# Optimization experiments

Measured on AMD Instinct MI355X. Metric: run time of the kernel, lower is better.

Reference implementation:

```python
import jax, jax.numpy as jnp
import numpy as np
from functools import partial

IMG, P, C, E, DEPTH, H, FE, NCLS = 224, 16, 3, 768, 12, 12, 4, 1000
B = 32
NP = (IMG // P) ** 2          # 196 patches
N = NP + 1                    # +cls token
HD = E // H                   # 64
FF = FE * E                   # 3072
EPS = 1e-5


def setup_inputs() -> dict:
    key = jax.random.key(0)
    ks = iter(jax.random.split(key, 32))
    r = lambda shape, s=0.02: (jax.random.normal(next(ks), shape, jnp.float32) * s)
    inp = {
        "x": jax.random.normal(next(ks), (B, C, IMG, IMG), jnp.float32),
        "conv_w": r((E, C, P, P)),              # OIHW
        "conv_b": r((E,)),
        "cls_token": r((1, 1, E)),
        "pos_emb": r((1, N, E)),
        # stacked per-layer params; Linear weights stored as [in, out]
        "Wq": r((DEPTH, E, E)), "Wk": r((DEPTH, E, E)), "Wv": r((DEPTH, E, E)),
        "Wo": r((DEPTH, E, E)), "bo": r((DEPTH, E)),
        "ln1_g": jnp.ones((DEPTH, E)), "ln1_b": jnp.zeros((DEPTH, E)),
        "W1": r((DEPTH, E, FF)), "b1": r((DEPTH, FF)),
        "W2": r((DEPTH, FF, E)), "b2": r((DEPTH, E)),
        "ln2_g": jnp.ones((DEPTH, E)), "ln2_b": jnp.zeros((DEPTH, E)),
        "head_g": jnp.ones((E,)), "head_b": jnp.zeros((E,)),
        "head_W": r((E, NCLS)), "head_bias": r((NCLS,)),
    }
    return inp


def _ln(x, g, b):
    m = jnp.mean(x, axis=-1, keepdims=True)
    v = jnp.var(x, axis=-1, keepdims=True)
    return (x - m) * jax.lax.rsqrt(v + EPS) * g + b


def _block(h, p):
    Wq, Wk, Wv, Wo, bo, g1, bn1, W1, b1, W2, b2, g2, bn2 = p
    b, n, _ = h.shape
    q = (h @ Wq).reshape(b, n, H, HD)
    k = (h @ Wk).reshape(b, n, H, HD)
    v = (h @ Wv).reshape(b, n, H, HD)
    # NOTE: original scales by sqrt(embed_size), not sqrt(head_dim)
    energy = jnp.einsum("bqhd,bkhd->bhqk", q, k) / jnp.sqrt(jnp.float32(E))
    attn = jax.nn.softmax(energy, axis=-1)
    out = jnp.einsum("bhqk,bkhd->bqhd", attn, v).reshape(b, n, E)
    out = out @ Wo + bo
    x = _ln(out + h, g1, bn1)
    f = jax.nn.relu(x @ W1 + b1) @ W2 + b2
    return _ln(f + x, g2, bn2), None


def reference(x, conv_w, conv_b, cls_token, pos_emb, Wq, Wk, Wv, Wo, bo,
              ln1_g, ln1_b, W1, b1, W2, b2, ln2_g, ln2_b,
              head_g, head_b, head_W, head_bias):
    # patch embedding: strided conv == non-overlapping patch projection
    h = jax.lax.conv_general_dilated(
        x, conv_w, window_strides=(P, P), padding="VALID",
        dimension_numbers=("NCHW", "OIHW", "NCHW"))
    h = h + conv_b[None, :, None, None]
    h = h.reshape(B, E, NP).transpose(0, 2, 1)          # [B, NP, E]
    cls = jnp.broadcast_to(cls_token, (B, 1, E))
    h = jnp.concatenate([cls, h], axis=1) + pos_emb      # [B, N, E]
    params = (Wq, Wk, Wv, Wo, bo, ln1_g, ln1_b, W1, b1, W2, b2, ln2_g, ln2_b)
    h, _ = jax.lax.scan(_block, h, params)
    cls_final = h[:, 0]
    return _ln(cls_final, head_g, head_b) @ head_W + head_bias
```

## Files before the change

kernel.cpp:

```cpp
#include <hip/hip_runtime.h>

#define NTOK 197
#define BATCH 32
#define ROWS (BATCH*NTOK)
#define EMB 768
#define FFDIM 3072
#define NHEAD 12
#define HDIM 64
#define NPAD 224

typedef __bf16 bf16x8_t __attribute__((ext_vector_type(8)));
typedef float f32x4 __attribute__((ext_vector_type(4)));
typedef unsigned short u16;
typedef u16 u16x4 __attribute__((ext_vector_type(4)));

__device__ __forceinline__ u16 f2b(float f) {
  union { float f; unsigned int u; } v; v.f = f;
  unsigned int r = v.u + 0x7fffu + ((v.u >> 16) & 1u);
  return (u16)(r >> 16);
}
__device__ __forceinline__ void gload16(const void* g, void* l) {
  __builtin_amdgcn_global_load_lds((const __attribute__((address_space(1))) void*)g,
                                   (__attribute__((address_space(3))) void*)l, 16, 0, 0);
}
__device__ __forceinline__ float wred_sum(float v) {
#pragma unroll
  for (int o = 32; o > 0; o >>= 1) v += __shfl_xor(v, o);
  return v;
}

__device__ __forceinline__ void xcd_swz(int& bx, int& by) {
  const int gx = gridDim.x;
  const int nwg = gx * gridDim.y;
  const int orig = by * gx + bx;
  const int q = nwg >> 3, r = nwg & 7;
  const int xcd = orig & 7, idx = orig >> 3;
  const int wg = (xcd < r ? xcd * (q + 1) : r * (q + 1) + (xcd - r) * q) + idx;
  by = wg / gx; bx = wg % gx;
}

template <bool HAS_BIAS, bool RELU, bool ADD_RES, bool OUT_BF16>
__global__ __launch_bounds__(256)
void gemm_bt(const u16* __restrict__ A, const u16* __restrict__ Bt, void* __restrict__ C,
             const float* __restrict__ bias, const float* __restrict__ res,
             int M, int N, int K) {
  __shared__ __align__(16) char lds[2][16384];
  const int tid = threadIdx.x;
  const int lane = tid & 63;
  const int wid = tid >> 6;
  const int wm = wid >> 1, wn = wid & 1;
  int bxs = blockIdx.x, bys = blockIdx.y;
  xcd_swz(bxs, bys);
  const int bm = bys * 128, bn = bxs * 128;
  const int r15 = lane & 15, khi = lane >> 4;

  f32x4 acc[4][4] = {};
  const int nk = K >> 5;

  auto stage = [&](int buf, int kt) {
    const int k0 = kt * 32 + khi * 8;
#pragma unroll
    for (int i = 0; i < 4; ++i) {
      int s = wid * 4 + i;
      char* ldst = &lds[buf][s * 1024];
      const u16* g;
      if (s < 8) {
        int row = bm + s * 16 + r15; if (row >= M) row = M - 1;
        g = A + (size_t)row * K + k0;
      } else {
        int row = bn + (s - 8) * 16 + r15;
        g = Bt + (size_t)row * K + k0;
      }
      gload16(g, ldst);
    }
  };

  stage(0, 0);
  __syncthreads();
  for (int kt = 0; kt < nk; ++kt) {
    const int cur = kt & 1;
    if (kt + 1 < nk) stage(cur ^ 1, kt + 1);
    bf16x8_t a[4], b[4];
#pragma unroll
    for (int mt = 0; mt < 4; ++mt)
      a[mt] = *(const bf16x8_t*)&lds[cur][(wm * 4 + mt) * 1024 + lane * 16];
#pragma unroll
    for (int nt = 0; nt < 4; ++nt)
      b[nt] = *(const bf16x8_t*)&lds[cur][8192 + (wn * 4 + nt) * 1024 + lane * 16];
#pragma unroll
    for (int mt = 0; mt < 4; ++mt)
#pragma unroll
      for (int nt = 0; nt < 4; ++nt)
        acc[mt][nt] = __builtin_amdgcn_mfma_f32_16x16x32_bf16(a[mt], b[nt], acc[mt][nt], 0, 0, 0);
    __syncthreads();
  }

#pragma unroll
  for (int mt = 0; mt < 4; ++mt) {
#pragma unroll
    for (int nt = 0; nt < 4; ++nt) {
      const int col = bn + wn * 64 + nt * 16 + r15;
      float bv = 0.f;
      if (HAS_BIAS) bv = bias[col];
#pragma unroll
      for (int j = 0; j < 4; ++j) {
        const int row = bm + wm * 64 + mt * 16 + khi * 4 + j;
        if (row < M) {
          float v = acc[mt][nt][j] + bv;
          if (ADD_RES) v += res[(size_t)row * N + col];
          if (RELU) v = v > 0.f ? v : 0.f;
          if (OUT_BF16) ((u16*)C)[(size_t)row * N + col] = f2b(v);
          else          ((float*)C)[(size_t)row * N + col] = v;
        }
      }
    }
  }
}

template <bool HAS_BIAS, bool RELU, bool OUT_BF16>
__global__ __launch_bounds__(512)
void gemm_bt2(const u16* __restrict__ A, const u16* __restrict__ Bt, void* __restrict__ C,
              const float* __restrict__ bias, int M, int N, int K) {
  __shared__ __align__(16) char lds[2][24576];
  const int tid = threadIdx.x;
  const int lane = tid & 63;
  const int wid = tid >> 6;
  const int wm = wid >> 1, wn = wid & 1;
  int bxs = blockIdx.x, bys = blockIdx.y;
  xcd_swz(bxs, bys);
  const int bm = bys * 256, bn = bxs * 128;
  const int r15 = lane & 15, khi = lane >> 4;

  f32x4 acc[4][4] = {};
  const int nk = K >> 5;

  auto stage = [&](int buf, int kt) {
    const int k0 = kt * 32 + khi * 8;
#pragma unroll
    for (int i = 0; i < 3; ++i) {
      int s = wid * 3 + i;
      char* ldst = &lds[buf][s * 1024];
      const u16* g;
      if (s < 16) {
        int row = bm + s * 16 + r15; if (row >= M) row = M - 1;
        g = A + (size_t)row * K + k0;
      } else {
        int row = bn + (s - 16) * 16 + r15;
        g = Bt + (size_t)row * K + k0;
      }
      gload16(g, ldst);
    }
  };

  stage(0, 0);
  stage(1, 1);
  for (int kt = 0; kt < nk; ++kt) {
    const int cur = kt & 1;
    if (kt + 1 < nk) { asm volatile("s_waitcnt vmcnt(3)" ::: "memory"); }
    else             { asm volatile("s_waitcnt vmcnt(0)" ::: "memory"); }
    __builtin_amdgcn_sched_barrier(0);
    __builtin_amdgcn_s_barrier();
    bf16x8_t a[4], b[4];
#pragma unroll
    for (int mt = 0; mt < 4; ++mt)
      a[mt] = *(const bf16x8_t*)&lds[cur][(wm * 4 + mt) * 1024 + lane * 16];
#pragma unroll
    for (int nt = 0; nt < 4; ++nt)
      b[nt] = *(const bf16x8_t*)&lds[cur][16384 + (wn * 4 + nt) * 1024 + lane * 16];
#pragma unroll
    for (int mt = 0; mt < 4; ++mt)
#pragma unroll
      for (int nt = 0; nt < 4; ++nt)
        acc[mt][nt] = __builtin_amdgcn_mfma_f32_16x16x32_bf16(a[mt], b[nt], acc[mt][nt], 0, 0, 0);
    asm volatile("s_waitcnt lgkmcnt(0)" ::: "memory");
    __builtin_amdgcn_sched_barrier(0);
    __builtin_amdgcn_s_barrier();
    if (kt + 2 < nk) stage(cur, kt + 2);
  }

#pragma unroll
  for (int mt = 0; mt < 4; ++mt) {
#pragma unroll
    for (int nt = 0; nt < 4; ++nt) {
      const int col = bn + wn * 64 + nt * 16 + r15;
      float bv = 0.f;
      if (HAS_BIAS) bv = bias[col];
#pragma unroll
      for (int j = 0; j < 4; ++j) {
        const int row = bm + wm * 64 + mt * 16 + khi * 4 + j;
        if (row < M) {
          float v = acc[mt][nt][j] + bv;
          if (RELU) v = v > 0.f ? v : 0.f;
          if (OUT_BF16) ((u16*)C)[(size_t)row * N + col] = f2b(v);
          else          ((float*)C)[(size_t)row * N + col] = v;
        }
      }
    }
  }
}

template <int NSK>
__global__ __launch_bounds__(256)
void gemm_bt_sk(const u16* __restrict__ A, const u16* __restrict__ Bt,
                float* __restrict__ P0, float* __restrict__ P1, float* __restrict__ P2,
                int M, int N, int K) {
  __shared__ __align__(16) char lds[2][16384];
  const int tid = threadIdx.x;
  const int lane = tid & 63;
  const int wid = tid >> 6;
  const int wm = wid >> 1, wn = wid & 1;
  int bxs = blockIdx.x, bys = blockIdx.y;
  xcd_swz(bxs, bys);
  const int bm = bys * 128, bn = bxs * 128;
  const int r15 = lane & 15, khi = lane >> 4;
  const int Kh = K / NSK;
  const int kbase = blockIdx.z * Kh;
  float* __restrict__ C = (blockIdx.z == 0) ? P0 : (blockIdx.z == 1 ? P1 : P2);

  f32x4 acc[4][4] = {};
  const int nk = Kh >> 5;

  auto stage = [&](int buf, int kt) {
    const int k0 = kbase + kt * 32 + khi * 8;
#pragma unroll
    for (int i = 0; i < 4; ++i) {
      int s = wid * 4 + i;
      char* ldst = &lds[buf][s * 1024];
      const u16* g;
      if (s < 8) {
        int row = bm + s * 16 + r15; if (row >= M) row = M - 1;
        g = A + (size_t)row * K + k0;
      } else {
        int row = bn + (s - 8) * 16 + r15;
        g = Bt + (size_t)row * K + k0;
      }
      gload16(g, ldst);
    }
  };

  stage(0, 0);
  stage(1, 1);
  for (int kt = 0; kt < nk; ++kt) {
    const int cur = kt & 1;
    if (kt + 1 < nk) { asm volatile("s_waitcnt vmcnt(4)" ::: "memory"); }
    else             { asm volatile("s_waitcnt vmcnt(0)" ::: "memory"); }
    __builtin_amdgcn_sched_barrier(0);
    __builtin_amdgcn_s_barrier();
    bf16x8_t a[4], b[4];
#pragma unroll
    for (int mt = 0; mt < 4; ++mt)
      a[mt] = *(const bf16x8_t*)&lds[cur][(wm * 4 + mt) * 1024 + lane * 16];
#pragma unroll
    for (int nt = 0; nt < 4; ++nt)
      b[nt] = *(const bf16x8_t*)&lds[cur][8192 + (wn * 4 + nt) * 1024 + lane * 16];
#pragma unroll
    for (int mt = 0; mt < 4; ++mt)
#pragma unroll
      for (int nt = 0; nt < 4; ++nt)
        acc[mt][nt] = __builtin_amdgcn_mfma_f32_16x16x32_bf16(a[mt], b[nt], acc[mt][nt], 0, 0, 0);
    asm volatile("s_waitcnt lgkmcnt(0)" ::: "memory");
    __builtin_amdgcn_sched_barrier(0);
    __builtin_amdgcn_s_barrier();
    if (kt + 2 < nk) stage(cur, kt + 2);
  }

#pragma unroll
  for (int mt = 0; mt < 4; ++mt) {
#pragma unroll
    for (int nt = 0; nt < 4; ++nt) {
      const int col = bn + wn * 64 + nt * 16 + r15;
#pragma unroll
      for (int j = 0; j < 4; ++j) {
        const int row = bm + wm * 64 + mt * 16 + khi * 4 + j;
        if (row < M) C[(size_t)row * N + col] = acc[mt][nt][j];
      }
    }
  }
}

__global__ __launch_bounds__(256)
void ln_red(const float* __restrict__ P0, const float* __restrict__ P1,
            const float* __restrict__ P2,
            const float* __restrict__ bias, const float* __restrict__ res,
            const float* __restrict__ g, const float* __restrict__ bv,
            float* __restrict__ o32, u16* __restrict__ obf) {
  const int row = blockIdx.x;
  const size_t b4 = (size_t)row * 192;
  const int tid = threadIdx.x;
  f32x4 vv = {0.f, 0.f, 0.f, 0.f};
  float ls = 0.f, lq = 0.f;
  if (tid < 192) {
    f32x4 a = ((const f32x4*)P0)[b4 + tid];
    f32x4 b = ((const f32x4*)P1)[b4 + tid];
    f32x4 p = ((const f32x4*)P2)[b4 + tid];
    f32x4 c = ((const f32x4*)res)[b4 + tid];
    f32x4 d = ((const f32x4*)bias)[tid];
    vv = a + b + p + c + d;
    ls = vv[0] + vv[1] + vv[2] + vv[3];
    lq = vv[0]*vv[0] + vv[1]*vv[1] + vv[2]*vv[2] + vv[3]*vv[3];
  }
  float s = wred_sum(ls);
  float s2 = wred_sum(lq);
  __shared__ float rs[4], rq[4];
  const int wv = tid >> 6, lane = tid & 63;
  if (lane == 0) { rs[wv] = s; rq[wv] = s2; }
  __syncthreads();
  float S1 = rs[0] + rs[1] + rs[2] + rs[3];
  float S2 = rq[0] + rq[1] + rq[2] + rq[3];
  float mean = S1 * (1.0f / 768.0f);
  float var = S2 * (1.0f / 768.0f) - mean * mean;
  float inv = rsqrtf(var + 1e-5f);
  if (tid < 192) {
    f32x4 gg = ((const f32x4*)g)[tid];
    f32x4 bb = ((const f32x4*)bv)[tid];
    f32x4 y;
    u16x4 ob;
#pragma unroll
    for (int k = 0; k < 4; ++k) {
      y[k] = (vv[k] - mean) * inv * gg[k] + bb[k];
      ob[k] = f2b(y[k]);
    }
    ((f32x4*)o32)[b4 + tid] = y;
    ((u16x4*)obf)[b4 + tid] = ob;
  }
}

__global__ void prep_layer(const float* __restrict__ Wq, const float* __restrict__ Wk,
                           const float* __restrict__ Wv, const float* __restrict__ Wo,
                           const float* __restrict__ W1, const float* __restrict__ W2,
                           u16* __restrict__ qkvT, u16* __restrict__ woT,
                           u16* __restrict__ w1T, u16* __restrict__ w2T) {
  __shared__ float tbuf[32][33];
  const int t = blockIdx.x;
  const float* src; u16* dst; int K, N, nt, kt;
  if (t < 2304) {
    int seg = t / 576, r = t % 576;
    nt = r % 24; kt = r / 24; K = 768; N = 768;
    if (seg == 0)      { src = Wq; dst = qkvT; }
    else if (seg == 1) { src = Wk; dst = qkvT + (size_t)768 * 768; }
    else if (seg == 2) { src = Wv; dst = qkvT + (size_t)2 * 768 * 768; }
    else               { src = Wo; dst = woT; }
  } else if (t < 4608) {
    int r = t - 2304; nt = r % 96; kt = r / 96;
    K = 768; N = 3072; src = W1; dst = w1T;
  } else {
    int r = t - 4608; nt = r % 24; kt = r / 24;
    K = 3072; N = 768; src = W2; dst = w2T;
  }
  const int n0 = nt * 32, k0 = kt * 32;
  const int tx = threadIdx.x, ty = threadIdx.y;
#pragma unroll
  for (int i = 0; i < 4; ++i)
    tbuf[ty + i * 8][tx] = src[(size_t)(k0 + ty + i * 8) * N + n0 + tx];
  __syncthreads();
#pragma unroll
  for (int i = 0; i < 4; ++i)
    dst[(size_t)(n0 + ty + i * 8) * K + k0 + tx] = f2b(tbuf[tx][ty + i * 8]);
}

__global__ void convert_bf(const float* __restrict__ s, u16* __restrict__ d, size_t n) {
  size_t i = (size_t)blockIdx.x * 256 + threadIdx.x;
  if (i < n) d[i] = f2b(s[i]);
}

__global__ void transpose_head(const float* __restrict__ src, float* __restrict__ dst) {
  __shared__ float tbuf[32][33];
  const int n0 = blockIdx.x * 32, k0 = blockIdx.y * 32;
  const int tx = threadIdx.x, ty = threadIdx.y;
#pragma unroll
  for (int i = 0; i < 4; ++i) {
    int k = k0 + ty + i * 8, n = n0 + tx;
    if (n < 1000) tbuf[ty + i * 8][tx] = src[(size_t)k * 1000 + n];
  }
  __syncthreads();
#pragma unroll
  for (int i = 0; i < 4; ++i) {
    int n = n0 + ty + i * 8, k = k0 + tx;
    if (n < 1000) dst[(size_t)n * 768 + k] = tbuf[tx][ty + i * 8];
  }
}

__global__ void im2col(const float* __restrict__ x, u16* __restrict__ A) {
  size_t idx = (size_t)blockIdx.x * 256 + threadIdx.x;
  if (idx >= (size_t)6272 * 768) return;
  int k = (int)(idx % 768); size_t row = idx / 768;
  int b = (int)(row / 196), p = (int)(row % 196);
  int py = p / 14, px = p % 14;
  int c = k >> 8, rem = k & 255, ph = rem >> 4, pw = rem & 15;
  float v = x[(((size_t)b * 3 + c) * 224 + (py * 16 + ph)) * 224 + (px * 16 + pw)];
  A[idx] = f2b(v);
}

__global__ void assemble_h0(const float* __restrict__ pout, const float* __restrict__ cls,
                            const float* __restrict__ pos, float* __restrict__ h32,
                            u16* __restrict__ hbf) {
  const int row = blockIdx.x;
  const int b = row / NTOK, n = row % NTOK;
  for (int c = threadIdx.x; c < EMB; c += 256) {
    float v;
    if (n == 0) v = cls[c] + pos[c];
    else v = pout[((size_t)b * 196 + (n - 1)) * EMB + c] + pos[(size_t)n * EMB + c];
    h32[(size_t)row * EMB + c] = v;
    hbf[(size_t)row * EMB + c] = f2b(v);
  }
}

__global__ void build_vT(const u16* __restrict__ qkv, u16* __restrict__ vT) {
  size_t idx = (size_t)blockIdx.x * 256 + threadIdx.x;
  if (idx >= (size_t)384 * HDIM * NPAD) return;
  int nn = (int)(idx % NPAD); size_t t = idx / NPAD;
  int d = (int)(t % HDIM); int bh = (int)(t / HDIM);
  int b = bh / NHEAD, h = bh % NHEAD;
  u16 v = 0;
  if (nn < NTOK) v = qkv[((size_t)b * NTOK + nn) * 2304 + 1536 + h * HDIM + d];
  vT[idx] = v;
}

__global__ __launch_bounds__(256)
void attn_sm(const u16* __restrict__ qkv, u16* __restrict__ P) {
  __shared__ __align__(16) char kf[13 * 2 * 1024];
  __shared__ __align__(16) char qf[2 * 2 * 1024];
  __shared__ float S[32][NPAD];
  const int bh = blockIdx.y;
  const int b = bh / NHEAD, h = bh % NHEAD;
  const int qb = blockIdx.x;
  const int tid = threadIdx.x, lane = tid & 63, wid = tid >> 6;
  const int r15 = lane & 15, khi = lane >> 4;

  const u16* qbase = qkv + (size_t)b * NTOK * 2304 + h * HDIM;
  const u16* kbase = qbase + 768;

  for (int i = wid; i < 26; i += 4) {
    int sub = i >> 1, ks = i & 1;
    int row = sub * 16 + r15; if (row > 196) row = 196;
    gload16(kbase + (size_t)row * 2304 + ks * 32 + khi * 8, &kf[(size_t)i * 1024]);
  }
  {
    int i = wid;
    int sub = i >> 1, ks = i & 1;
    int row = qb * 32 + sub * 16 + r15; if (row > 196) row = 196;
    gload16(qbase + (size_t)row * 2304 + ks * 32 + khi * 8, &qf[(size_t)i * 1024]);
  }
  __syncthreads();

  const float scale = 0.03608439182435161f;
  for (int t = wid; t < 26; t += 4) {
    int qi = t / 13, ki = t % 13;
    f32x4 acc = {};
    bf16x8_t aq0 = *(const bf16x8_t*)&qf[(qi * 2 + 0) * 1024 + lane * 16];
    bf16x8_t aq1 = *(const bf16x8_t*)&qf[(qi * 2 + 1) * 1024 + lane * 16];
    bf16x8_t bk0 = *(const bf16x8_t*)&kf[(ki * 2 + 0) * 1024 + lane * 16];
    bf16x8_t bk1 = *(const bf16x8_t*)&kf[(ki * 2 + 1) * 1024 + lane * 16];
    acc = __builtin_amdgcn_mfma_f32_16x16x32_bf16(aq0, bk0, acc, 0, 0, 0);
    acc = __builtin_amdgcn_mfma_f32_16x16x32_bf16(aq1, bk1, acc, 0, 0, 0);
#pragma unroll
    for (int j = 0; j < 4; ++j) S[qi * 16 + khi * 4 + j][ki * 16 + r15] = acc[j] * scale;
  }
  __syncthreads();

  for (int i = 0; i < 8; ++i) {
    const int r = wid * 8 + i;
    const int q = qb * 32 + r;
    if (q > 196) continue;
    float vals[4]; float m = -1e30f;
#pragma unroll
    for (int c = 0; c < 4; ++c) {
      int col = lane + c * 64;
      float v = (col < NTOK) ? S[r][col] : -1e30f;
      vals[c] = v; m = fmaxf(m, v);
    }
#pragma unroll
    for (int o = 32; o > 0; o >>= 1) m = fmaxf(m, __shfl_xor(m, o));
    float s = 0.f;
#pragma unroll
    for (int c = 0; c < 4; ++c) { float e = __expf(vals[c] - m); vals[c] = e; s += e; }
    s = wred_sum(s);
    float inv = 1.f / s;
    u16* prow = P + ((size_t)bh * NTOK + q) * NPAD;
#pragma unroll
    for (int c = 0; c < 4; ++c) {
      int col = lane + c * 64;
      if (col < NPAD) prow[col] = f2b(vals[c] * inv);
    }
  }
}

__global__ __launch_bounds__(256)
void attn_pv(const u16* __restrict__ P, const u16* __restrict__ vT, u16* __restrict__ out) {
  __shared__ __align__(16) char lds[2][17 * 1024];
  const int bh = blockIdx.x;
  const int b = bh / NHEAD, h = bh % NHEAD;
  const int tid = threadIdx.x, lane = tid & 63, wid = tid >> 6;
  const int r15 = lane & 15, khi = lane >> 4;
  const u16* Pb = P + (size_t)bh * NTOK * NPAD;
  const u16* Vb = vT + (size_t)bh * HDIM * NPAD;

  f32x4 acc[4][4] = {};
  auto stage = [&](int buf, int kt) {
    for (int i = wid; i < 17; i += 4) {
      const u16* g;
      if (i < 13) { int row = i * 16 + r15; if (row > 196) row = 196;
                    g = Pb + (size_t)row * NPAD + kt * 32 + khi * 8; }
      else        { int row = (i - 13) * 16 + r15;
                    g = Vb + (size_t)row * NPAD + kt * 32 + khi * 8; }
      gload16(g, &lds[buf][i * 1024]);
    }
  };
  stage(0, 0);
  __syncthreads();
  for (int kt = 0; kt < 7; ++kt) {
    const int cur = kt & 1;
    if (kt + 1 < 7) stage(cur ^ 1, kt + 1);
    bf16x8_t bb[4];
#pragma unroll
    for (int di = 0; di < 4; ++di)
      bb[di] = *(const bf16x8_t*)&lds[cur][(13 + di) * 1024 + lane * 16];
#pragma unroll
    for (int s = 0; s < 4; ++s) {
      int qi = wid + s * 4;
      if (qi < 13) {
        bf16x8_t a = *(const bf16x8_t*)&lds[cur][qi * 1024 + lane * 16];
#pragma unroll
        for (int di = 0; di < 4; ++di)
          acc[s][di] = __builtin_amdgcn_mfma_f32_16x16x32_bf16(a, bb[di], acc[s][di], 0, 0, 0);
      }
    }
    __syncthreads();
  }
#pragma unroll
  for (int s = 0; s < 4; ++s) {
    int qi = wid + s * 4;
    if (qi >= 13) continue;
#pragma unroll
    for (int di = 0; di < 4; ++di) {
      int col = h * HDIM + di * 16 + r15;
#pragma unroll
      for (int j = 0; j < 4; ++j) {
        int q = qi * 16 + khi * 4 + j;
        if (q < NTOK) out[((size_t)b * NTOK + q) * EMB + col] = f2b(acc[s][di][j]);
      }
    }
  }
}

__global__ __launch_bounds__(256)
void ln_cls(const float* __restrict__ h32, const float* __restrict__ hg,
            const float* __restrict__ hb, float* __restrict__ cls_ln) {
  const int b = blockIdx.x;
  const float* xr = h32 + (size_t)b * NTOK * EMB;
  const int tid = threadIdx.x;
  float v0 = xr[tid], v1 = xr[tid + 256], v2 = xr[tid + 512];
  float s = wred_sum(v0 + v1 + v2);
  float s2 = wred_sum(v0 * v0 + v1 * v1 + v2 * v2);
  __shared__ float rs[4], rq[4];
  const int wid = tid >> 6, lane = tid & 63;
  if (lane == 0) { rs[wid] = s; rq[wid] = s2; }
  __syncthreads();
  float S1 = rs[0] + rs[1] + rs[2] + rs[3];
  float S2 = rq[0] + rq[1] + rq[2] + rq[3];
  float mean = S1 * (1.0f / 768.0f);
  float var = S2 * (1.0f / 768.0f) - mean * mean;
  float inv = rsqrtf(var + 1e-5f);
  cls_ln[(size_t)b * EMB + tid]       = (v0 - mean) * inv * hg[tid]       + hb[tid];
  cls_ln[(size_t)b * EMB + tid + 256] = (v1 - mean) * inv * hg[tid + 256] + hb[tid + 256];
  cls_ln[(size_t)b * EMB + tid + 512] = (v2 - mean) * inv * hg[tid + 512] + hb[tid + 512];
}

__global__ __launch_bounds__(256)
void head2(const float* __restrict__ cls_ln, const float* __restrict__ hWT,
           const float* __restrict__ bias, float* __restrict__ out) {
  __shared__ float t[EMB];
  const int b = blockIdx.y;
  const int tid = threadIdx.x, lane = tid & 63, wid = tid >> 6;
  t[tid] = cls_ln[(size_t)b * EMB + tid];
  t[tid + 256] = cls_ln[(size_t)b * EMB + tid + 256];
  t[tid + 512] = cls_ln[(size_t)b * EMB + tid + 512];
  __syncthreads();
  const int j = blockIdx.x * 4 + wid;
  const float* wr = hWT + (size_t)j * EMB;
  float a = 0.f;
#pragma unroll
  for (int i = 0; i < 12; ++i) {
    int e = lane + i * 64;
    a += t[e] * wr[e];
  }
  a = wred_sum(a);
  if (lane == 0) out[(size_t)b * 1000 + j] = a + bias[j];
}

extern "C" void kernel_launch(void* const* d_in, const int* in_sizes, int n_in,
                              void* d_out, int out_size, void* d_ws, size_t ws_size,
                              hipStream_t stream) {
  const float* x      = (const float*)d_in[0];
  const float* conv_w = (const float*)d_in[1];
  const float* conv_b = (const float*)d_in[2];
  const float* cls    = (const float*)d_in[3];
  const float* pos    = (const float*)d_in[4];
  const float* Wq     = (const float*)d_in[5];
  const float* Wk     = (const float*)d_in[6];
  const float* Wv     = (const float*)d_in[7];
  const float* Wo     = (const float*)d_in[8];
  const float* bo     = (const float*)d_in[9];
  const float* ln1g   = (const float*)d_in[10];
  const float* ln1b   = (const float*)d_in[11];
  const float* W1     = (const float*)d_in[12];
  const float* b1     = (const float*)d_in[13];
  const float* W2     = (const float*)d_in[14];
  const float* b2     = (const float*)d_in[15];
  const float* ln2g   = (const float*)d_in[16];
  const float* ln2b   = (const float*)d_in[17];
  const float* hg     = (const float*)d_in[18];
  const float* hb     = (const float*)d_in[19];
  const float* hW     = (const float*)d_in[20];
  const float* hbias  = (const float*)d_in[21];

  char* ws = (char*)d_ws;
  size_t off = 0;
  auto alloc = [&](size_t bytes) { void* p = ws + off; off += (bytes + 255) & ~(size_t)255; return p; };

  u16*   qkvT = (u16*)alloc((size_t)2304 * 768 * 2);
  u16*   woTl = (u16*)alloc((size_t)768 * 768 * 2);
  u16*   w1Tl = (u16*)alloc((size_t)3072 * 768 * 2);
  u16*   w2Tl = (u16*)alloc((size_t)768 * 3072 * 2);
  u16*   cw   = (u16*)alloc((size_t)768 * 768 * 2);
  float* h32  = (float*)alloc((size_t)ROWS * EMB * 4);
  u16*   hbf  = (u16*)alloc((size_t)ROWS * EMB * 2);
  u16*   qkv  = (u16*)alloc((size_t)ROWS * 2304 * 2);
  u16*   vT   = (u16*)alloc((size_t)384 * HDIM * NPAD * 2);
  char*  big  = (char*)alloc(2 * (size_t)ROWS * EMB * 4);
  u16*   Pbuf = (u16*)big;
  u16*   mid  = (u16*)big;
  float* pout = (float*)big;
  float* woP0 = (float*)big;
  float* woP1 = (float*)(big + (size_t)ROWS * EMB * 4);
  u16*   att  = (u16*)alloc((size_t)ROWS * EMB * 2);
  u16*   xbf  = att;
  float* ybuf = (float*)alloc((size_t)ROWS * EMB * 4);
  float* x32  = (float*)alloc((size_t)ROWS * EMB * 4);
  float* hWT  = (float*)alloc((size_t)1000 * EMB * 4);
  float* clsl = (float*)alloc((size_t)32 * EMB * 4);
  u16*   Apatch = qkv;
  float* woP2 = ybuf;
  float* f2P0 = (float*)qkv;
  float* f2P1 = ybuf;
  float* f2P2 = h32;

  if (off > ws_size) return;

  convert_bf<<<2304, 256, 0, stream>>>(conv_w, cw, (size_t)768 * 768);
  transpose_head<<<dim3(32, 24), dim3(32, 8), 0, stream>>>(hW, hWT);
  im2col<<<18816, 256, 0, stream>>>(x, Apatch);
  gemm_bt<true, false, false, false><<<dim3(6, 49), 256, 0, stream>>>(Apatch, cw, pout, conv_b, nullptr, 6272, 768, 768);
  assemble_h0<<<ROWS, 256, 0, stream>>>(pout, cls, pos, h32, hbf);

  for (int l = 0; l < 12; ++l) {
    const size_t wo = (size_t)l * 768 * 768;
    prep_layer<<<6912, dim3(32, 8), 0, stream>>>(
        Wq + wo, Wk + wo, Wv + wo, Wo + wo,
        W1 + (size_t)l * 768 * 3072, W2 + (size_t)l * 3072 * 768,
        qkvT, woTl, w1Tl, w2Tl);
    gemm_bt2<false, false, true><<<dim3(18, 25), 512, 0, stream>>>(
        hbf, qkvT, qkv, nullptr, ROWS, 2304, 768);
    build_vT<<<21504, 256, 0, stream>>>(qkv, vT);
    attn_sm<<<dim3(7, 384), 256, 0, stream>>>(qkv, Pbuf);
    attn_pv<<<384, 256, 0, stream>>>(Pbuf, vT, att);
    gemm_bt_sk<3><<<dim3(6, 50, 3), 256, 0, stream>>>(att, woTl, woP0, woP1, woP2, ROWS, 768, 768);
    ln_red<<<ROWS, 256, 0, stream>>>(woP0, woP1, woP2, bo + (size_t)l * 768, h32,
                                     ln1g + (size_t)l * 768, ln1b + (size_t)l * 768, x32, xbf);
    gemm_bt2<true, true, true><<<dim3(24, 25), 512, 0, stream>>>(
        xbf, w1Tl, mid, b1 + (size_t)l * 3072, ROWS, FFDIM, 768);
    gemm_bt_sk<3><<<dim3(6, 50, 3), 256, 0, stream>>>(mid, w2Tl, f2P0, f2P1, f2P2, ROWS, 768, FFDIM);
    ln_red<<<ROWS, 256, 0, stream>>>(f2P0, f2P1, f2P2, b2 + (size_t)l * 768, x32,
                                     ln2g + (size_t)l * 768, ln2b + (size_t)l * 768, h32, hbf);
  }

  ln_cls<<<32, 256, 0, stream>>>(h32, hg, hb, clsl);
  head2<<<dim3(250, 32), 256, 0, stream>>>(clsl, hWT, hbias, (float*)d_out);
}
```

Baseline: 3.857 ms.

## Batch weight prep for all layers in one launch and merge attention query blocks

All 12 layers' weights are converted and transposed to bf16 in a single 2D-grid prep_layer launch up front, provided the workspace can hold them, instead of one launch per layer. This removes 11 launches and lets the conversion run as one large kernel. The attention softmax kernel now loops over several query blocks per workgroup, loading K into LDS once per 3-4 query blocks instead of once per block, which cuts redundant K loads but reduces the grid from 7x384 to 2x384 blocks. It needs roughly 170MB of extra workspace and falls back to per-layer prep otherwise.

```diff
diff --git a/kernel.cpp b/kernel.cpp
--- a/kernel.cpp
+++ b/kernel.cpp
@@ -325,12 +325,16 @@
   }
 }
 
-__global__ void prep_layer(const float* __restrict__ Wq, const float* __restrict__ Wk,
-                           const float* __restrict__ Wv, const float* __restrict__ Wo,
-                           const float* __restrict__ W1, const float* __restrict__ W2,
-                           u16* __restrict__ qkvT, u16* __restrict__ woT,
-                           u16* __restrict__ w1T, u16* __restrict__ w2T) {
+__global__ void prep_layer(const float* Wq, const float* Wk,
+                           const float* Wv, const float* Wo,
+                           const float* W1, const float* W2,
+                           u16* qkvT, u16* woT, u16* w1T, u16* w2T) {
   __shared__ float tbuf[32][33];
+  const size_t l = blockIdx.y;
+  Wq += l * 768 * 768;  Wk += l * 768 * 768;  Wv += l * 768 * 768;  Wo += l * 768 * 768;
+  W1 += l * 768 * 3072; W2 += l * 3072 * 768;
+  qkvT += l * 2304 * 768; woT += l * 768 * 768;
+  w1T  += l * 3072 * 768; w2T += l * 768 * 3072;
   const int t = blockIdx.x;
   const float* src; u16* dst; int K, N, nt, kt;
   if (t < 2304) {
@@ -417,13 +421,15 @@
 }
 
 __global__ __launch_bounds__(256)
-void attn_sm(const u16* __restrict__ qkv, u16* __restrict__ P) {
-  __shared__ __align__(16) char kf[13 * 2 * 1024];
-  __shared__ __align__(16) char qf[2 * 2 * 1024];
+void attn_sm2(const u16* __restrict__ qkv, u16* __restrict__ P) {
+  __shared__ __align__(16) char kf[26 * 1024];
+  __shared__ __align__(16) char qf[4 * 1024];
   __shared__ float S[32][NPAD];
   const int bh = blockIdx.y;
   const int b = bh / NHEAD, h = bh % NHEAD;
-  const int qb = blockIdx.x;
+  const int z = blockIdx.x;
+  const int qb0 = z * 4;
+  const int nqb = z ? 3 : 4;
   const int tid = threadIdx.x, lane = tid & 63, wid = tid >> 6;
   const int r15 = lane & 15, khi = lane >> 4;
 
@@ -435,52 +441,56 @@
     int row = sub * 16 + r15; if (row > 196) row = 196;
     gload16(kbase + (size_t)row * 2304 + ks * 32 + khi * 8, &kf[(size_t)i * 1024]);
   }
-  {
-    int i = wid;
-    int sub = i >> 1, ks = i & 1;
-    int row = qb * 32 + sub * 16 + r15; if (row > 196) row = 196;
-    gload16(qbase + (size_t)row * 2304 + ks * 32 + khi * 8, &qf[(size_t)i * 1024]);
-  }
-  __syncthreads();
 
   const float scale = 0.03608439182435161f;
-  for (int t = wid; t < 26; t += 4) {
-    int qi = t / 13, ki = t % 13;
-    f32x4 acc = {};
-    bf16x8_t aq0 = *(const bf16x8_t*)&qf[(qi * 2 + 0) * 1024 + lane * 16];
-    bf16x8_t aq1 = *(const bf16x8_t*)&qf[(qi * 2 + 1) * 1024 + lane * 16];
-    bf16x8_t bk0 = *(const bf16x8_t*)&kf[(ki * 2 + 0) * 1024 + lane * 16];
-    bf16x8_t bk1 = *(const bf16x8_t*)&kf[(ki * 2 + 1) * 1024 + lane * 16];
-    acc = __builtin_amdgcn_mfma_f32_16x16x32_bf16(aq0, bk0, acc, 0, 0, 0);
-    acc = __builtin_amdgcn_mfma_f32_16x16x32_bf16(aq1, bk1, acc, 0, 0, 0);
-#pragma unroll
-    for (int j = 0; j < 4; ++j) S[qi * 16 + khi * 4 + j][ki * 16 + r15] = acc[j] * scale;
-  }
-  __syncthreads();
-
-  for (int i = 0; i < 8; ++i) {
-    const int r = wid * 8 + i;
-    const int q = qb * 32 + r;
-    if (q > 196) continue;
-    float vals[4]; float m = -1e30f;
-#pragma unroll
-    for (int c = 0; c < 4; ++c) {
-      int col = lane + c * 64;
-      float v = (col < NTOK) ? S[r][col] : -1e30f;
-      vals[c] = v; m = fmaxf(m, v);
-    }
-#pragma unroll
-    for (int o = 32; o > 0; o >>= 1) m = fmaxf(m, __shfl_xor(m, o));
-    float s = 0.f;
-#pragma unroll
-    for (int c = 0; c < 4; ++c) { float e = __expf(vals[c] - m); vals[c] = e; s += e; }
-    s = wred_sum(s);
-    float inv = 1.f / s;
-    u16* prow = P + ((size_t)bh * NTOK + q) * NPAD;
-#pragma unroll
-    for (int c = 0; c < 4; ++c) {
-      int col = lane + c * 64;
-      if (col < NPAD) prow[col] = f2b(vals[c] * inv);
+  for (int qq = 0; qq < nqb; ++qq) {
+    const int qb = qb0 + qq;
+    {
+      int i = wid;
+      int sub = i >> 1, ks = i & 1;
+      int row = qb * 32 + sub * 16 + r15; if (row > 196) row = 196;
+      gload16(qbase + (size_t)row * 2304 + ks * 32 + khi * 8, &qf[(size_t)i * 1024]);
+    }
+    __syncthreads();
+
+    for (int t = wid; t < 26; t += 4) {
+      int qi = t / 13, ki = t % 13;
+      f32x4 acc = {};
+      bf16x8_t aq0 = *(const bf16x8_t*)&qf[(qi * 2 + 0) * 1024 + lane * 16];
+      bf16x8_t aq1 = *(const bf16x8_t*)&qf[(qi * 2 + 1) * 1024 + lane * 16];
+      bf16x8_t bk0 = *(const bf16x8_t*)&kf[(ki * 2 + 0) * 1024 + lane * 16];
+      bf16x8_t bk1 = *(const bf16x8_t*)&kf[(ki * 2 + 1) * 1024 + lane * 16];
+      acc = __builtin_amdgcn_mfma_f32_16x16x32_bf16(aq0, bk0, acc, 0, 0, 0);
+      acc = __builtin_amdgcn_mfma_f32_16x16x32_bf16(aq1, bk1, acc, 0, 0, 0);
+#pragma unroll
+      for (int j = 0; j < 4; ++j) S[qi * 16 + khi * 4 + j][ki * 16 + r15] = acc[j] * scale;
+    }
+    __syncthreads();
+
+    for (int i = 0; i < 8; ++i) {
+      const int r = wid * 8 + i;
+      const int q = qb * 32 + r;
+      if (q > 196) continue;
+      float vals[4]; float m = -1e30f;
+#pragma unroll
+      for (int c = 0; c < 4; ++c) {
+        int col = lane + c * 64;
+        float v = (col < NTOK) ? S[r][col] : -1e30f;
+        vals[c] = v; m = fmaxf(m, v);
+      }
+#pragma unroll
+      for (int o = 32; o > 0; o >>= 1) m = fmaxf(m, __shfl_xor(m, o));
+      float s = 0.f;
+#pragma unroll
+      for (int c = 0; c < 4; ++c) { float e = __expf(vals[c] - m); vals[c] = e; s += e; }
+      s = wred_sum(s);
+      float inv = 1.f / s;
+      u16* prow = P + ((size_t)bh * NTOK + q) * NPAD;
+#pragma unroll
+      for (int c = 0; c < 4; ++c) {
+        int col = lane + c * 64;
+        if (col < NPAD) prow[col] = f2b(vals[c] * inv);
+      }
     }
   }
 }
@@ -647,29 +657,49 @@
 
   if (off > ws_size) return;
 
+  size_t offBase = off;
+  u16* qkvTA = (u16*)alloc((size_t)12 * 2304 * 768 * 2);
+  u16* woTA  = (u16*)alloc((size_t)12 * 768 * 768 * 2);
+  u16* w1TA  = (u16*)alloc((size_t)12 * 3072 * 768 * 2);
+  u16* w2TA  = (u16*)alloc((size_t)12 * 768 * 3072 * 2);
+  bool bigW = (off <= ws_size);
+  if (!bigW) off = offBase;
+
   convert_bf<<<2304, 256, 0, stream>>>(conv_w, cw, (size_t)768 * 768);
   transpose_head<<<dim3(32, 24), dim3(32, 8), 0, stream>>>(hW, hWT);
+  if (bigW)
+    prep_layer<<<dim3(6912, 12), dim3(32, 8), 0, stream>>>(
+        Wq, Wk, Wv, Wo, W1, W2, qkvTA, woTA, w1TA, w2TA);
   im2col<<<18816, 256, 0, stream>>>(x, Apatch);
   gemm_bt<true, false, false, false><<<dim3(6, 49), 256, 0, stream>>>(Apatch, cw, pout, conv_b, nullptr, 6272, 768, 768);
   assemble_h0<<<ROWS, 256, 0, stream>>>(pout, cls, pos, h32, hbf);
 
   for (int l = 0; l < 12; ++l) {
     const size_t wo = (size_t)l * 768 * 768;
-    prep_layer<<<6912, dim3(32, 8), 0, stream>>>(
-        Wq + wo, Wk + wo, Wv + wo, Wo + wo,
-        W1 + (size_t)l * 768 * 3072, W2 + (size_t)l * 3072 * 768,
-        qkvT, woTl, w1Tl, w2Tl);
+    const u16 *qT, *woT_, *w1T_, *w2T_;
+    if (bigW) {
+      qT   = qkvTA + (size_t)l * 2304 * 768;
+      woT_ = woTA  + (size_t)l * 768 * 768;
+      w1T_ = w1TA  + (size_t)l * 3072 * 768;
+      w2T_ = w2TA  + (size_t)l * 768 * 3072;
+    } else {
+      prep_layer<<<dim3(6912, 1), dim3(32, 8), 0, stream>>>(
+          Wq + wo, Wk + wo, Wv + wo, Wo + wo,
+          W1 + (size_t)l * 768 * 3072, W2 + (size_t)l * 3072 * 768,
+          qkvT, woTl, w1Tl, w2Tl);
+      qT = qkvT; woT_ = woTl; w1T_ = w1Tl; w2T_ = w2Tl;
+    }
     gemm_bt2<false, false, true><<<dim3(18, 25), 512, 0, stream>>>(
-        hbf, qkvT, qkv, nullptr, ROWS, 2304, 768);
+        hbf, qT, qkv, nullptr, ROWS, 2304, 768);
     build_vT<<<21504, 256, 0, stream>>>(qkv, vT);
-    attn_sm<<<dim3(7, 384), 256, 0, stream>>>(qkv, Pbuf);
+    attn_sm2<<<dim3(2, 384), 256, 0, stream>>>(qkv, Pbuf);
     attn_pv<<<384, 256, 0, stream>>>(Pbuf, vT, att);
-    gemm_bt_sk<3><<<dim3(6, 50, 3), 256, 0, stream>>>(att, woTl, woP0, woP1, woP2, ROWS, 768, 768);
+    gemm_bt_sk<3><<<dim3(6, 50, 3), 256, 0, stream>>>(att, woT_, woP0, woP1, woP2, ROWS, 768, 768);
     ln_red<<<ROWS, 256, 0, stream>>>(woP0, woP1, woP2, bo + (size_t)l * 768, h32,
                                      ln1g + (size_t)l * 768, ln1b + (size_t)l * 768, x32, xbf);
     gemm_bt2<true, true, true><<<dim3(24, 25), 512, 0, stream>>>(
-        xbf, w1Tl, mid, b1 + (size_t)l * 3072, ROWS, FFDIM, 768);
-    gemm_bt_sk<3><<<dim3(6, 50, 3), 256, 0, stream>>>(mid, w2Tl, f2P0, f2P1, f2P2, ROWS, 768, FFDIM);
+        xbf, w1T_, mid, b1 + (size_t)l * 3072, ROWS, FFDIM, 768);
+    gemm_bt_sk<3><<<dim3(6, 50, 3), 256, 0, stream>>>(mid, w2T_, f2P0, f2P1, f2P2, ROWS, 768, FFDIM);
     ln_red<<<ROWS, 256, 0, stream>>>(f2P0, f2P1, f2P2, b2 + (size_t)l * 768, x32,
                                      ln2g + (size_t)l * 768, ln2b + (size_t)l * 768, h32, hbf);
   }
```

Result: slower. 4.077 ms (+5.7%).
